# Kernel optimization log

Hardware: AMD Instinct MI355X
Metric: run time of the kernel (lower is better)

Reference implementation:

```python
import jax, jax.numpy as jnp
import numpy as np


def _conv3d(x, w):
    # x: [N, C, D, H, W], w: [O, I, K, K, K] -> [N, O, D', H', W'] VALID conv
    return jax.lax.conv_general_dilated(
        x, w, window_strides=(1, 1, 1), padding='VALID',
        dimension_numbers=('NCDHW', 'OIDHW', 'NCDHW'))


def conv4d(x, w):
    # x: [B, C, D1, D2, D3, D4]; w: [O, I, K1, K2, K3, K4]
    # Decompose 4D conv as a sum over K1 taps of 3D convs; the sliced D1
    # window is folded into the batch dimension so XLA's 3D conv does the work.
    B, C, D1, D2, D3, D4 = x.shape
    O, I, K1, K2, K3, K4 = w.shape
    D1o = D1 - K1 + 1
    out = None
    for i in range(K1):  # small fixed loop over kernel taps (K1=3)
        xs = jax.lax.dynamic_slice_in_dim(x, i, D1o, axis=2)      # [B,C,D1o,D2,D3,D4]
        xs = xs.transpose(0, 2, 1, 3, 4, 5).reshape(B * D1o, C, D2, D3, D4)
        y = _conv3d(xs, w[:, :, i])                                # [B*D1o,O,d2,d3,d4]
        out = y if out is None else out + y
    d2, d3, d4 = out.shape[2], out.shape[3], out.shape[4]
    out = out.reshape(B, D1o, O, d2, d3, d4).transpose(0, 2, 1, 3, 4, 5)
    return out  # [B, O, D1o, d2, d3, d4]


def setup_inputs() -> dict:
    key = jax.random.key(0)
    k1, k2 = jax.random.split(key)
    pic_in = jax.random.normal(k1, (2, 16, 8, 8, 64, 64), dtype=jnp.float32)
    # convNd weight: [out_channels, in_channels, K, K, K, K], no bias
    weight = jax.random.normal(k2, (32, 16, 3, 3, 3, 3), dtype=jnp.float32) * 0.05
    return {"pic_in": pic_in, "weight": weight}


def reference(pic_in, weight):
    # ConvKernel.forward: 4D conv (stride 1, padding 0, no bias) + ReLU
    return jax.nn.relu(conv4d(pic_in, weight))
```

## Files before the change

kernel.cpp:

```cpp
#include <hip/hip_runtime.h>


typedef __attribute__((ext_vector_type(8))) __bf16 bf16x8;
typedef __attribute__((ext_vector_type(16))) float f32x16;

#define CSTRIDE 262144

#define WT_OFF 0
#define XB_OFF 131072

__global__ __launch_bounds__(256) void prep(const float* __restrict__ x,
                                            const float* __restrict__ w,
                                            unsigned char* __restrict__ ws) {
  int blk = blockIdx.x;
  if (blk < 512) {
    __bf16* xb = (__bf16*)(ws + XB_OFF);
    int n = blk * 256 + threadIdx.x;
    int cg = n & 15;
    int d3 = (n >> 4) & 63;
    int d2 = (n >> 10) & 7;
    int d1 = (n >> 13) & 7;
    int b = n >> 16;
    const float* gx =
        x + ((((b * 16) * 8 + d1) * 8 + d2) * 64 + d3) * 64 + cg * 4;
    float4 v[16];
#pragma unroll
    for (int c = 0; c < 16; ++c)
      v[c] = *(const float4*)(gx + (size_t)c * CSTRIDE);
    __bf16* row = xb + ((((b * 8 + d1) * 8 + d2) * 64 + d3) * 1024);
#pragma unroll
    for (int ch = 0; ch < 2; ++ch) {
#pragma unroll
      for (int j = 0; j < 4; ++j) {
        bf16x8 o;
#pragma unroll
        for (int cc = 0; cc < 8; ++cc)
          o[cc] = (__bf16)(((const float*)&v[ch * 8 + cc])[j]);
        *(bf16x8*)(row + ch * 512 + (cg * 4 + j) * 8) = o;
      }
    }
  } else {
    int o = blk - 512;
    __bf16* wT = (__bf16*)(ws + WT_OFF);
#pragma unroll
    for (int base = 0; base < 1296; base += 256) {
      int idx = base + threadIdx.x;
      if (idx < 1296) {
        int c = idx / 81, t = idx % 81;
        wT[t * 512 + o * 16 + c] = (__bf16)w[o * 1296 + idx];
      }
    }
  }
}

__global__ __launch_bounds__(64, 3) void conv_mfma(
    const unsigned char* __restrict__ ws, float* __restrict__ out) {
  const unsigned char* wTb = ws + WT_OFF;
  const unsigned char* xbb = ws + XB_OFF;

  int bid = blockIdx.x;
  int c3 = bid & 15;
  int th = (bid >> 4) & 1;
  int t = bid >> 5;
  int e2 = t % 6;
  t /= 6;
  int e1 = t % 6;
  int b = t / 6;
  int r0 = c3 * 4;

  int lane = threadIdx.x;
  int m32 = lane & 31;
  int half = lane >> 5;

  int aoff = half * 1024 + (th * 32 + m32) * 16;
  int woff = m32 * 32 + half * 16;

  f32x16 acc[4];
#pragma unroll
  for (int i = 0; i < 4; ++i)
#pragma unroll
    for (int r = 0; r < 16; ++r) acc[i][r] = 0.f;

  for (int k1 = 0; k1 < 3; ++k1) {
    for (int k2 = 0; k2 < 3; ++k2) {
      const unsigned char* abase =
          xbb +
          (size_t)(((b * 8 + e1 + k1) * 8 + e2 + k2) * 64 + r0) * 2048 + aoff;
      const unsigned char* wbase = wTb + (k1 * 3 + k2) * 9216 + woff;
#pragma unroll
      for (int k4 = 0; k4 < 3; ++k4) {
        bf16x8 arow[6];
#pragma unroll
        for (int j = 0; j < 6; ++j)
          arow[j] = *(const bf16x8*)(abase + j * 2048 + k4 * 16);
#pragma unroll
        for (int k3 = 0; k3 < 3; ++k3) {
          bf16x8 bf = *(const bf16x8*)(wbase + (k3 * 3 + k4) * 1024);
#pragma unroll
          for (int i = 0; i < 4; ++i)
            acc[i] = __builtin_amdgcn_mfma_f32_32x32x16_bf16(arow[i + k3], bf,
                                                             acc[i], 0, 0, 0);
        }
      }
    }
  }

  __shared__ float sc[32 * 33];
  int e4 = th * 32 + m32;
  size_t obase_be = ((size_t)b * 32 * 36 + e1 * 6 + e2) * 3844;
#pragma unroll
  for (int i = 0; i < 4; ++i) {
    int e3 = r0 + i;
    if (e3 >= 62) break;
    __syncthreads();
#pragma unroll
    for (int r = 0; r < 16; ++r) {
      int m = (r & 3) + 8 * (r >> 2) + 4 * half;
      sc[m * 33 + m32] = acc[i][r];
    }
    __syncthreads();
#pragma unroll
    for (int it = 0; it < 16; ++it) {
      int o = it * 2 + half;
      float v = fmaxf(sc[m32 * 33 + o], 0.f);
      if (e4 < 62)
        out[obase_be + (size_t)o * 138384 + (size_t)e3 * 62 + e4] = v;
    }
  }
}

extern "C" void kernel_launch(void* const* d_in, const int* in_sizes, int n_in,
                              void* d_out, int out_size, void* d_ws,
                              size_t ws_size, hipStream_t stream) {
  const float* x = (const float*)d_in[0];
  const float* w = (const float*)d_in[1];
  float* out = (float*)d_out;
  unsigned char* ws = (unsigned char*)d_ws;
  prep<<<dim3(544), dim3(256), 0, stream>>>(x, w, ws);
  conv_mfma<<<dim3(2 * 6 * 6 * 2 * 16), dim3(64), 0, stream>>>(ws, out);
}
```

Measured before the change: 127.2 us.

## Split K1/K2 reduction across waves with LDS reduction in 4-wave blocks

Each block now holds 4 waves instead of 1. Two of the waves cover the two e4 halves and two cover a split of the 9 (k1,k2) taps, 4 and 5 per wave. The partial accumulators are summed through shared memory before ReLU and the store. The block order is also remapped so that adjacent blocks share the same row chunk, which should improve L2 reuse. The goal is more waves in flight for latency hiding, at the cost of an uneven 4/5 tap split, extra LDS traffic and barriers.

Measured after the change: 132.9 us. 4.5% more time.

```diff
diff --git a/kernel.cpp b/kernel.cpp
--- a/kernel.cpp
+++ b/kernel.cpp
@@ -53,22 +53,23 @@
   }
 }
 
-__global__ __launch_bounds__(64, 3) void conv_mfma(
+__global__ __launch_bounds__(256, 4) void conv_mfma(
     const unsigned char* __restrict__ ws, float* __restrict__ out) {
   const unsigned char* wTb = ws + WT_OFF;
   const unsigned char* xbb = ws + XB_OFF;
 
   int bid = blockIdx.x;
-  int c3 = bid & 15;
-  int th = (bid >> 4) & 1;
-  int t = bid >> 5;
-  int e2 = t % 6;
-  t /= 6;
-  int e1 = t % 6;
-  int b = t / 6;
-  int r0 = c3 * 4;
+  int g = bid % 72;
+  int chunk = bid / 72;
+  int b = g / 36;
+  int e1 = (g / 6) % 6;
+  int e2 = g % 6;
+  int r0 = chunk * 4;
 
-  int lane = threadIdx.x;
+  int lane = threadIdx.x & 63;
+  int wave = threadIdx.x >> 6;
+  int th = wave & 1;
+  int kp = wave >> 1;
   int m32 = lane & 31;
   int half = lane >> 5;
 
@@ -81,50 +82,64 @@
 #pragma unroll
     for (int r = 0; r < 16; ++r) acc[i][r] = 0.f;
 
-  for (int k1 = 0; k1 < 3; ++k1) {
-    for (int k2 = 0; k2 < 3; ++k2) {
-      const unsigned char* abase =
-          xbb +
-          (size_t)(((b * 8 + e1 + k1) * 8 + e2 + k2) * 64 + r0) * 2048 + aoff;
-      const unsigned char* wbase = wTb + (k1 * 3 + k2) * 9216 + woff;
+  int p0 = kp ? 4 : 0;
+  int p1 = kp ? 9 : 4;
+  for (int p = p0; p < p1; ++p) {
+    int k1 = (p >= 3) + (p >= 6);
+    int k2 = p - k1 * 3;
+    const unsigned char* abase =
+        xbb + (size_t)(((b * 8 + e1 + k1) * 8 + e2 + k2) * 64 + r0) * 2048 +
+        aoff;
+    const unsigned char* wbase = wTb + p * 9216 + woff;
 #pragma unroll
-      for (int k4 = 0; k4 < 3; ++k4) {
-        bf16x8 arow[6];
+    for (int k4 = 0; k4 < 3; ++k4) {
+      bf16x8 arow[6];
 #pragma unroll
-        for (int j = 0; j < 6; ++j)
-          arow[j] = *(const bf16x8*)(abase + j * 2048 + k4 * 16);
+      for (int j = 0; j < 6; ++j)
+        arow[j] = *(const bf16x8*)(abase + j * 2048 + k4 * 16);
 #pragma unroll
-        for (int k3 = 0; k3 < 3; ++k3) {
-          bf16x8 bf = *(const bf16x8*)(wbase + (k3 * 3 + k4) * 1024);
+      for (int k3 = 0; k3 < 3; ++k3) {
+        bf16x8 bf = *(const bf16x8*)(wbase + (k3 * 3 + k4) * 1024);
 #pragma unroll
-          for (int i = 0; i < 4; ++i)
-            acc[i] = __builtin_amdgcn_mfma_f32_32x32x16_bf16(arow[i + k3], bf,
-                                                             acc[i], 0, 0, 0);
-        }
+        for (int i = 0; i < 4; ++i)
+          acc[i] = __builtin_amdgcn_mfma_f32_32x32x16_bf16(arow[i + k3], bf,
+                                                           acc[i], 0, 0, 0);
       }
     }
   }
 
-  __shared__ float sc[32 * 33];
+  __shared__ float sc[2][32 * 33];
+  float* s = sc[th];
   int e4 = th * 32 + m32;
-  size_t obase_be = ((size_t)b * 32 * 36 + e1 * 6 + e2) * 3844;
+  size_t obase =
+      ((((size_t)b * 32) * 6 + e1) * 6 + e2) * 3844;
 #pragma unroll
   for (int i = 0; i < 4; ++i) {
-    int e3 = r0 + i;
-    if (e3 >= 62) break;
     __syncthreads();
+    if (kp == 1) {
 #pragma unroll
-    for (int r = 0; r < 16; ++r) {
-      int m = (r & 3) + 8 * (r >> 2) + 4 * half;
-      sc[m * 33 + m32] = acc[i][r];
+      for (int r = 0; r < 16; ++r) {
+        int m = (r & 3) + 8 * (r >> 2) + 4 * half;
+        s[m * 33 + m32] = acc[i][r];
+      }
     }
     __syncthreads();
+    if (kp == 0) {
 #pragma unroll
-    for (int it = 0; it < 16; ++it) {
-      int o = it * 2 + half;
-      float v = fmaxf(sc[m32 * 33 + o], 0.f);
-      if (e4 < 62)
-        out[obase_be + (size_t)o * 138384 + (size_t)e3 * 62 + e4] = v;
+      for (int r = 0; r < 16; ++r) {
+        int m = (r & 3) + 8 * (r >> 2) + 4 * half;
+        s[m * 33 + m32] += acc[i][r];
+      }
+      int e3 = r0 + i;
+      if (e3 < 62) {
+#pragma unroll
+        for (int it = 0; it < 16; ++it) {
+          int o = it * 2 + half;
+          float v = fmaxf(s[m32 * 33 + o], 0.f);
+          if (e4 < 62)
+            out[obase + (size_t)o * 138384 + (size_t)e3 * 62 + e4] = v;
+        }
+      }
     }
   }
 }
@@ -137,5 +152,5 @@
   float* out = (float*)d_out;
   unsigned char* ws = (unsigned char*)d_ws;
   prep<<<dim3(544), dim3(256), 0, stream>>>(x, w, ws);
-  conv_mfma<<<dim3(2 * 6 * 6 * 2 * 16), dim3(64), 0, stream>>>(ws, out);
+  conv_mfma<<<dim3(16 * 72), dim3(256), 0, stream>>>(ws, out);
 }
```
